# Optimization experiments

Measured on AMD Instinct MI355X. Metric: run time of the kernel, lower is better.

The kernel has to match this reference:

```python
import jax, jax.numpy as jnp
import numpy as np

N = 8192
D_IN = 1024
D_OUT = 1024


def setup_inputs() -> dict:
    key = jax.random.key(0)
    ks = jax.random.split(key, 7)
    s = 1.0 / np.sqrt(D_IN)
    return {
        "feat": jax.random.normal(ks[0], (N, D_IN), dtype=jnp.float32),
        "Wq": jax.random.uniform(ks[1], (D_IN, D_OUT), jnp.float32, -s, s),
        "bq": jax.random.uniform(ks[2], (D_OUT,), jnp.float32, -s, s),
        "Wk": jax.random.uniform(ks[3], (D_IN, D_OUT), jnp.float32, -s, s),
        "bk": jax.random.uniform(ks[4], (D_OUT,), jnp.float32, -s, s),
        "Wv": jax.random.uniform(ks[5], (D_IN, D_OUT), jnp.float32, -s, s),
        "bv": jax.random.uniform(ks[6], (D_OUT,), jnp.float32, -s, s),
    }


def reference(feat, Wq, bq, Wk, bk, Wv, bv):
    # eval mode: dropout(p=0.3, training=False) is identity
    q = feat @ Wq + bq          # [N, D_OUT]
    k = feat @ Wk + bk          # [N, D_OUT]
    v = feat @ Wv + bv          # [N, D_OUT]
    scale = 1.0 / jnp.sqrt(jnp.float32(D_OUT))
    scores = (q @ k.T) * scale  # [N, N]
    attn = jax.nn.softmax(scores, axis=1)
    return attn @ v             # [N, D_OUT]
```

## Files before the change

### kernel.cpp

```cpp
#include <hip/hip_runtime.h>
#include <hip/hip_bf16.h>
#include <stdint.h>

typedef __hip_bfloat16 bf16;
typedef __attribute__((ext_vector_type(8))) short short8;
typedef __attribute__((ext_vector_type(4))) float f32x4;

#define BM 128
#define BN 128

__device__ __forceinline__ unsigned short f2bf_bits(float x) {
    return __builtin_bit_cast(unsigned short, __float2bfloat16(x));
}

__device__ __forceinline__ void gload_lds16(const bf16* g, bf16* l) {
    __builtin_amdgcn_global_load_lds(
        (const __attribute__((address_space(1))) void*)(const void*)g,
        (__attribute__((address_space(3))) void*)(void*)l,
        16, 0, 0);
}

__global__ void cvt_f32_bf16_x4(const float* __restrict__ in, unsigned short* __restrict__ out, int n4) {
    int i = blockIdx.x * 256 + threadIdx.x;
    if (i < n4) {
        float4 v = reinterpret_cast<const float4*>(in)[i];
        ushort4 o;
        o.x = f2bf_bits(v.x); o.y = f2bf_bits(v.y);
        o.z = f2bf_bits(v.z); o.w = f2bf_bits(v.w);
        reinterpret_cast<ushort4*>(out)[i] = o;
    }
}

__global__ void wtrans_kernel(const float* __restrict__ W0, const float* __restrict__ W1,
                              const float* __restrict__ W2, bf16* __restrict__ Wt) {
    __shared__ float tile[32][33];
    const int z = blockIdx.z;
    const float* in = (z == 0) ? W0 : (z == 1) ? W1 : W2;
    bf16* out = Wt + (size_t)z * 1024 * 1024;
    const int bx = blockIdx.x, by = blockIdx.y, tx = threadIdx.x;
    for (int r = threadIdx.y; r < 32; r += 8)
        tile[r][tx] = in[(size_t)(by * 32 + r) * 1024 + bx * 32 + tx];
    __syncthreads();
    for (int r = threadIdx.y; r < 32; r += 8)
        out[(size_t)(bx * 32 + r) * 1024 + by * 32 + tx] = __float2bfloat16(tile[tx][r]);
}

__global__ void tpose_bf16(const bf16* __restrict__ in, bf16* __restrict__ out, int rows, int cols) {
    __shared__ bf16 tile[32][33];
    const int bx = blockIdx.x, by = blockIdx.y, tx = threadIdx.x;
    for (int r = threadIdx.y; r < 32; r += 8)
        tile[r][tx] = in[(size_t)(by * 32 + r) * cols + bx * 32 + tx];
    __syncthreads();
    for (int r = threadIdx.y; r < 32; r += 8)
        out[(size_t)(bx * 32 + r) * rows + by * 32 + tx] = tile[tx][r];
}

__global__ void scale_rows(float* __restrict__ out, const float* __restrict__ lsum) {
    int i = blockIdx.x * 256 + threadIdx.x;
    float4 v = reinterpret_cast<float4*>(out)[i];
    float inv = 1.0f / lsum[i >> 8];
    v.x *= inv; v.y *= inv; v.z *= inv; v.w *= inv;
    reinterpret_cast<float4*>(out)[i] = v;
}

template <int MODE, int KH>
__global__ __launch_bounds__(256, 2)
void gemm_bt(const bf16* __restrict__ A, const bf16* __restrict__ B,
             const float* __restrict__ b0, const float* __restrict__ b1,
             const float* __restrict__ b2, float* __restrict__ lsum,
             bf16* __restrict__ outb, float* __restrict__ outf,
             int M, int N, int K, int ldb, int ldout, float scale) {
    constexpr int BKT  = KH * 32;
    constexpr int TILE = 128 * 32;
    constexpr int SELEMS = (2 * KH * TILE < 9216) ? 9216 : 2 * KH * TILE;
    __shared__ bf16 smem[SELEMS];
    bf16* As = smem;
    bf16* Bs = smem + KH * TILE;

    const int tid  = threadIdx.x;
    const int lane = tid & 63;
    const int wave = tid >> 6;
    const int wm = wave & 1, wn = wave >> 1;
    const int l16  = lane & 15;
    const int quad = lane >> 4;
    const long bm0 = (long)blockIdx.x * BM;
    const long bn0 = (long)blockIdx.y * BN;

    const float* bias = nullptr;
    if (MODE == 0) {
        const int z = blockIdx.z;
        B    += (size_t)z * N * K;
        outb += (size_t)z * M * ldout;
        bias  = (z == 0) ? b0 : (z == 1) ? b1 : b2;
    }

    const int lrow = lane >> 2;
    const int lcol = (lane & 3) * 8;
    const bf16* gA[2][KH];
    const bf16* gB[2][KH];
    bf16* lA[2][KH];
    bf16* lB[2][KH];
#pragma unroll
    for (int u = 0; u < 2; u++)
#pragma unroll
        for (int h = 0; h < KH; h++) {
            gA[u][h] = A + (size_t)(bm0 + wave * 32 + u * 16 + lrow) * K + h * 32 + lcol;
            gB[u][h] = B + (size_t)(bn0 + wave * 32 + u * 16 + lrow) * ldb + h * 32 + lcol;
            lA[u][h] = As + h * TILE + (wave * 32 + u * 16) * 32;
            lB[u][h] = Bs + h * TILE + (wave * 32 + u * 16) * 32;
        }

    const bf16* Ard = As + (wm * 64 + l16) * 32 + quad * 8;
    const bf16* Brd = Bs + (wn * 64 + l16) * 32 + quad * 8;

    f32x4 acc[4][4];
    const f32x4 zero = {0.f, 0.f, 0.f, 0.f};
#pragma unroll
    for (int i = 0; i < 4; i++)
#pragma unroll
        for (int j = 0; j < 4; j++) acc[i][j] = zero;

    for (int k0 = 0; k0 < K; k0 += BKT) {
        __syncthreads();
#pragma unroll
        for (int u = 0; u < 2; u++)
#pragma unroll
            for (int h = 0; h < KH; h++) {
                gload_lds16(gA[u][h] + k0, lA[u][h]);
                gload_lds16(gB[u][h] + k0, lB[u][h]);
            }
        __syncthreads();
#pragma unroll
        for (int h = 0; h < KH; h++) {
            short8 af[4], bfr[4];
#pragma unroll
            for (int mi = 0; mi < 4; mi++)
                af[mi] = *reinterpret_cast<const short8*>(Ard + h * TILE + mi * 16 * 32);
#pragma unroll
            for (int ni = 0; ni < 4; ni++)
                bfr[ni] = *reinterpret_cast<const short8*>(Brd + h * TILE + ni * 16 * 32);
#pragma unroll
            for (int mi = 0; mi < 4; mi++)
#pragma unroll
                for (int ni = 0; ni < 4; ni++)
                    acc[mi][ni] = __builtin_amdgcn_mfma_f32_16x16x32_bf16(af[mi], bfr[ni], acc[mi][ni], 0, 0, 0);
        }
    }

    if (MODE == 0 || MODE == 1) {
        __syncthreads();
        bf16* eb = smem + wave * 1152;
        float bcol[4];
        if (MODE == 0) {
#pragma unroll
            for (int ni = 0; ni < 4; ni++) bcol[ni] = bias[bn0 + wn * 64 + l16 + ni * 16];
        }
#pragma unroll
        for (int mi = 0; mi < 4; mi++) {
#pragma unroll
            for (int r = 0; r < 4; r++) {
                float s = 0.f;
#pragma unroll
                for (int ni = 0; ni < 4; ni++) {
                    float v = acc[mi][ni][r];
                    if (MODE == 0) v += bcol[ni];
                    else { v = __expf(v * scale); s += v; }
                    eb[(quad * 4 + r) * 72 + ni * 16 + l16] = __float2bfloat16(v);
                }
                if (MODE == 1) {
                    s += __shfl_xor(s, 1);
                    s += __shfl_xor(s, 2);
                    s += __shfl_xor(s, 4);
                    s += __shfl_xor(s, 8);
                    if (l16 == 0) atomicAdd(&lsum[bm0 + wm * 64 + mi * 16 + quad * 4 + r], s);
                }
            }
            asm volatile("s_waitcnt lgkmcnt(0)" ::: "memory");
#pragma unroll
            for (int p = 0; p < 2; p++) {
                int r2 = p * 8 + (lane >> 3);
                int c2 = (lane & 7) * 8;
                short8 val = *reinterpret_cast<const short8*>(eb + r2 * 72 + c2);
                *reinterpret_cast<short8*>(
                    outb + (size_t)(bm0 + wm * 64 + mi * 16 + r2) * ldout + bn0 + wn * 64 + c2) = val;
            }
            asm volatile("s_waitcnt lgkmcnt(0)" ::: "memory");
        }
    } else {
        const int rb2 = wm * 64 + quad * 4;
        const int cb2 = wn * 64 + l16;
#pragma unroll
        for (int mi = 0; mi < 4; mi++)
#pragma unroll
            for (int r = 0; r < 4; r++) {
                long row = bm0 + rb2 + mi * 16 + r;
                float mul = (MODE == 3) ? 1.0f / lsum[row] : 0.f;
#pragma unroll
                for (int ni = 0; ni < 4; ni++) {
                    long col = bn0 + cb2 + ni * 16;
                    if (MODE == 3) outf[row * ldout + col] = acc[mi][ni][r] * mul;
                    else           outf[row * ldout + col] += acc[mi][ni][r];
                }
            }
    }
}

extern "C" void kernel_launch(void* const* d_in, const int* in_sizes, int n_in,
                              void* d_out, int out_size, void* d_ws, size_t ws_size,
                              hipStream_t stream) {
    const float* feat = (const float*)d_in[0];
    const float* Wq   = (const float*)d_in[1];
    const float* bqv  = (const float*)d_in[2];
    const float* Wk   = (const float*)d_in[3];
    const float* bkv  = (const float*)d_in[4];
    const float* Wv   = (const float*)d_in[5];
    const float* bvv  = (const float*)d_in[6];
    float* outp = (float*)d_out;

    const int M = 8192, D = 1024;
    char* ws = (char*)d_ws;
    size_t off = 0;
    auto carve = [&](size_t bytes) -> char* {
        char* r = ws + off;
        off += (bytes + 255) & ~(size_t)255;
        return r;
    };
    bf16* featb = (bf16*)carve((size_t)M * D * 2);
    bf16* Wbt   = (bf16*)carve((size_t)3 * D * D * 2);
    bf16* qkv   = (bf16*)carve((size_t)3 * M * D * 2);
    float* lsum = (float*)carve((size_t)M * 4);
    bf16* vbt   = featb;
    size_t avail = (ws_size > off) ? ws_size - off : 0;

    int C;
    if      (avail >= (size_t)M * M * 2)    C = M;
    else if (avail >= (size_t)M * 4096 * 2) C = 4096;
    else if (avail >= (size_t)M * 2048 * 2) C = 2048;
    else                                    C = 1024;
    bf16* Pc = (bf16*)carve((size_t)M * C * 2);

    {
        int n4 = M * D / 4;
        cvt_f32_bf16_x4<<<dim3((n4 + 255) / 256), dim3(256), 0, stream>>>(feat, (unsigned short*)featb, n4);
    }
    wtrans_kernel<<<dim3(32, 32, 3), dim3(32, 8), 0, stream>>>(Wq, Wk, Wv, Wbt);
    gemm_bt<0, 1><<<dim3(M / 128, D / 128, 3), dim3(256), 0, stream>>>(
        featb, Wbt, bqv, bkv, bvv, nullptr, qkv, nullptr, M, D, D, D, D, 1.0f);
    tpose_bf16<<<dim3(D / 32, M / 32), dim3(32, 8), 0, stream>>>(qkv + (size_t)2 * M * D, vbt, M, D);
    hipMemsetAsync(lsum, 0, (size_t)M * 4, stream);

    const float scale = 0.03125f;
    bf16* qb = qkv;
    bf16* kb = qkv + (size_t)M * D;
    if (C == M) {
        gemm_bt<1, 1><<<dim3(M / 128, M / 128), dim3(256), 0, stream>>>(
            qb, kb, nullptr, nullptr, nullptr, lsum, Pc, nullptr, M, M, D, D, M, scale);
        gemm_bt<3, 2><<<dim3(M / 128, D / 128), dim3(256), 0, stream>>>(
            Pc, vbt, nullptr, nullptr, nullptr, lsum, nullptr, outp, M, D, M, M, D, 0.f);
    } else {
        hipMemsetAsync(outp, 0, (size_t)M * D * 4, stream);
        for (int c = 0; c < M / C; c++) {
            gemm_bt<1, 1><<<dim3(M / 128, C / 128), dim3(256), 0, stream>>>(
                qb, kb + (size_t)c * C * D, nullptr, nullptr, nullptr, lsum, Pc, nullptr,
                M, C, D, D, C, scale);
            gemm_bt<2, 2><<<dim3(M / 128, D / 128), dim3(256), 0, stream>>>(
                Pc, vbt + (size_t)c * C, nullptr, nullptr, nullptr, nullptr, nullptr, outp,
                M, D, C, M, D, 0.f);
        }
        scale_rows<<<dim3(M * D / 4 / 256), dim3(256), 0, stream>>>(outp, lsum);
    }
}
```

Baseline: 477.5 us.

## Compute Q·K^T scores with FP8 MFMA, storing Q and K as FP8

The QKV projection now writes Q and K as FP8 (e4m3) instead of bf16, and a new kernel computes the N×N score GEMM with the scaled 16x16x128 f8f6f4 MFMA. Exp, row-sum and bf16 output are fused into its epilogue as before. This aims to halve operand bytes and double matrix throughput for the largest GEMM. The cost is lower precision in the attention scores, which could hurt accuracy given unscaled FP8 conversion.

```diff
diff --git a/kernel.cpp b/kernel.cpp
--- a/kernel.cpp
+++ b/kernel.cpp
@@ -5,6 +5,7 @@
 typedef __hip_bfloat16 bf16;
 typedef __attribute__((ext_vector_type(8))) short short8;
 typedef __attribute__((ext_vector_type(4))) float f32x4;
+typedef __attribute__((ext_vector_type(8))) int i32x8;
 
 #define BM 128
 #define BN 128
@@ -13,11 +14,24 @@
     return __builtin_bit_cast(unsigned short, __float2bfloat16(x));
 }
 
-__device__ __forceinline__ void gload_lds16(const bf16* g, bf16* l) {
+__device__ __forceinline__ float bfbits2f(unsigned short b) {
+    return __builtin_bit_cast(float, (unsigned)b << 16);
+}
+
+__device__ __forceinline__ void gload_lds16(const void* g, void* l) {
     __builtin_amdgcn_global_load_lds(
-        (const __attribute__((address_space(1))) void*)(const void*)g,
-        (__attribute__((address_space(3))) void*)(void*)l,
+        (const __attribute__((address_space(1))) void*)g,
+        (__attribute__((address_space(3))) void*)l,
         16, 0, 0);
+}
+
+__device__ __forceinline__ i32x8 ldfrag32(const uint8_t* p) {
+    int4 a = *reinterpret_cast<const int4*>(p);
+    int4 b = *reinterpret_cast<const int4*>(p + 16);
+    i32x8 r;
+    r[0] = a.x; r[1] = a.y; r[2] = a.z; r[3] = a.w;
+    r[4] = b.x; r[5] = b.y; r[6] = b.z; r[7] = b.w;
+    return r;
 }
 
 __global__ void cvt_f32_bf16_x4(const float* __restrict__ in, unsigned short* __restrict__ out, int n4) {
@@ -69,8 +83,8 @@
              const float* __restrict__ b0, const float* __restrict__ b1,
              const float* __restrict__ b2, float* __restrict__ lsum,
              bf16* __restrict__ outb, float* __restrict__ outf,
+             uint8_t* __restrict__ qk8,
              int M, int N, int K, int ldb, int ldout, float scale) {
-    constexpr int BKT  = KH * 32;
     constexpr int TILE = 128 * 32;
     constexpr int SELEMS = (2 * KH * TILE < 9216) ? 9216 : 2 * KH * TILE;
     __shared__ bf16 smem[SELEMS];
@@ -87,11 +101,11 @@
     const long bn0 = (long)blockIdx.y * BN;
 
     const float* bias = nullptr;
+    int z = 0;
     if (MODE == 0) {
-        const int z = blockIdx.z;
-        B    += (size_t)z * N * K;
-        outb += (size_t)z * M * ldout;
-        bias  = (z == 0) ? b0 : (z == 1) ? b1 : b2;
+        z = blockIdx.z;
+        B   += (size_t)z * N * K;
+        bias = (z == 0) ? b0 : (z == 1) ? b1 : b2;
     }
 
     const int lrow = lane >> 2;
@@ -120,7 +134,7 @@
 #pragma unroll
         for (int j = 0; j < 4; j++) acc[i][j] = zero;
 
-    for (int k0 = 0; k0 < K; k0 += BKT) {
+    for (int k0 = 0; k0 < K; k0 += KH * 32) {
         __syncthreads();
 #pragma unroll
         for (int u = 0; u < 2; u++)
@@ -147,42 +161,43 @@
         }
     }
 
-    if (MODE == 0 || MODE == 1) {
+    if (MODE == 0) {
         __syncthreads();
         bf16* eb = smem + wave * 1152;
         float bcol[4];
-        if (MODE == 0) {
-#pragma unroll
-            for (int ni = 0; ni < 4; ni++) bcol[ni] = bias[bn0 + wn * 64 + l16 + ni * 16];
-        }
+#pragma unroll
+        for (int ni = 0; ni < 4; ni++) bcol[ni] = bias[bn0 + wn * 64 + l16 + ni * 16];
 #pragma unroll
         for (int mi = 0; mi < 4; mi++) {
 #pragma unroll
-            for (int r = 0; r < 4; r++) {
-                float s = 0.f;
-#pragma unroll
-                for (int ni = 0; ni < 4; ni++) {
-                    float v = acc[mi][ni][r];
-                    if (MODE == 0) v += bcol[ni];
-                    else { v = __expf(v * scale); s += v; }
-                    eb[(quad * 4 + r) * 72 + ni * 16 + l16] = __float2bfloat16(v);
-                }
-                if (MODE == 1) {
-                    s += __shfl_xor(s, 1);
-                    s += __shfl_xor(s, 2);
-                    s += __shfl_xor(s, 4);
-                    s += __shfl_xor(s, 8);
-                    if (l16 == 0) atomicAdd(&lsum[bm0 + wm * 64 + mi * 16 + quad * 4 + r], s);
-                }
-            }
+            for (int r = 0; r < 4; r++)
+#pragma unroll
+                for (int ni = 0; ni < 4; ni++)
+                    eb[(quad * 4 + r) * 72 + ni * 16 + l16] =
+                        __float2bfloat16(acc[mi][ni][r] + bcol[ni]);
             asm volatile("s_waitcnt lgkmcnt(0)" ::: "memory");
 #pragma unroll
             for (int p = 0; p < 2; p++) {
                 int r2 = p * 8 + (lane >> 3);
                 int c2 = (lane & 7) * 8;
                 short8 val = *reinterpret_cast<const short8*>(eb + r2 * 72 + c2);
-                *reinterpret_cast<short8*>(
-                    outb + (size_t)(bm0 + wm * 64 + mi * 16 + r2) * ldout + bn0 + wn * 64 + c2) = val;
+                long row = bm0 + wm * 64 + mi * 16 + r2;
+                long col = bn0 + wn * 64 + c2;
+                if (z < 2) {
+                    unsigned lo = 0, hi = 0;
+                    lo = __builtin_amdgcn_cvt_pk_fp8_f32(bfbits2f((unsigned short)val[0]),
+                                                         bfbits2f((unsigned short)val[1]), lo, false);
+                    lo = __builtin_amdgcn_cvt_pk_fp8_f32(bfbits2f((unsigned short)val[2]),
+                                                         bfbits2f((unsigned short)val[3]), lo, true);
+                    hi = __builtin_amdgcn_cvt_pk_fp8_f32(bfbits2f((unsigned short)val[4]),
+                                                         bfbits2f((unsigned short)val[5]), hi, false);
+                    hi = __builtin_amdgcn_cvt_pk_fp8_f32(bfbits2f((unsigned short)val[6]),
+                                                         bfbits2f((unsigned short)val[7]), hi, true);
+                    int2 o; o.x = (int)lo; o.y = (int)hi;
+                    *reinterpret_cast<int2*>(qk8 + (size_t)z * M * ldout + row * ldout + col) = o;
+                } else {
+                    *reinterpret_cast<short8*>(outb + row * (size_t)ldout + col) = val;
+                }
             }
             asm volatile("s_waitcnt lgkmcnt(0)" ::: "memory");
         }
@@ -202,6 +217,106 @@
                     else           outf[row * ldout + col] += acc[mi][ni][r];
                 }
             }
+    }
+}
+
+__global__ __launch_bounds__(256, 2)
+void gemm_s_fp8(const uint8_t* __restrict__ A, const uint8_t* __restrict__ B,
+                float* __restrict__ lsum, bf16* __restrict__ outb,
+                int ldout, float scale) {
+    __shared__ uint8_t smem[32768];
+    uint8_t* As = smem;
+    uint8_t* Bs = smem + 16384;
+
+    const int tid  = threadIdx.x;
+    const int lane = tid & 63;
+    const int wave = tid >> 6;
+    const int wm = wave & 1, wn = wave >> 1;
+    const int l16  = lane & 15;
+    const int quad = lane >> 4;
+    const long bm0 = (long)blockIdx.x * BM;
+    const long bn0 = (long)blockIdx.y * BN;
+
+    const int lrow = lane >> 2;
+    const int lcol = (lane & 3) * 16;
+    const uint8_t* gA[2][2];
+    const uint8_t* gB[2][2];
+    uint8_t* lA[2][2];
+    uint8_t* lB[2][2];
+#pragma unroll
+    for (int u = 0; u < 2; u++)
+#pragma unroll
+        for (int h = 0; h < 2; h++) {
+            gA[u][h] = A + (size_t)(bm0 + wave * 32 + u * 16 + lrow) * 1024 + h * 64 + lcol;
+            gB[u][h] = B + (size_t)(bn0 + wave * 32 + u * 16 + lrow) * 1024 + h * 64 + lcol;
+            lA[u][h] = As + h * 8192 + (wave * 32 + u * 16) * 64;
+            lB[u][h] = Bs + h * 8192 + (wave * 32 + u * 16) * 64;
+        }
+
+    const uint8_t* Ard = As + (quad >> 1) * 8192 + (wm * 64 + l16) * 64 + (quad & 1) * 32;
+    const uint8_t* Brd = Bs + (quad >> 1) * 8192 + (wn * 64 + l16) * 64 + (quad & 1) * 32;
+
+    f32x4 acc[4][4];
+    const f32x4 zero = {0.f, 0.f, 0.f, 0.f};
+#pragma unroll
+    for (int i = 0; i < 4; i++)
+#pragma unroll
+        for (int j = 0; j < 4; j++) acc[i][j] = zero;
+
+    for (int k0 = 0; k0 < 1024; k0 += 128) {
+        __syncthreads();
+#pragma unroll
+        for (int u = 0; u < 2; u++)
+#pragma unroll
+            for (int h = 0; h < 2; h++) {
+                gload_lds16(gA[u][h] + k0, lA[u][h]);
+                gload_lds16(gB[u][h] + k0, lB[u][h]);
+            }
+        __syncthreads();
+        i32x8 af[4], bfr[4];
+#pragma unroll
+        for (int mi = 0; mi < 4; mi++)
+            af[mi] = ldfrag32(Ard + mi * 16 * 64);
+#pragma unroll
+        for (int ni = 0; ni < 4; ni++)
+            bfr[ni] = ldfrag32(Brd + ni * 16 * 64);
+#pragma unroll
+        for (int mi = 0; mi < 4; mi++)
+#pragma unroll
+            for (int ni = 0; ni < 4; ni++)
+                acc[mi][ni] = __builtin_amdgcn_mfma_scale_f32_16x16x128_f8f6f4(
+                    af[mi], bfr[ni], acc[mi][ni], 0, 0, 0, 0x7F7F7F7F, 0, 0x7F7F7F7F);
+    }
+
+    __syncthreads();
+    bf16* eb = reinterpret_cast<bf16*>(smem) + wave * 1152;
+#pragma unroll
+    for (int mi = 0; mi < 4; mi++) {
+#pragma unroll
+        for (int r = 0; r < 4; r++) {
+            float s = 0.f;
+#pragma unroll
+            for (int ni = 0; ni < 4; ni++) {
+                float e = __expf(acc[mi][ni][r] * scale);
+                s += e;
+                eb[(quad * 4 + r) * 72 + ni * 16 + l16] = __float2bfloat16(e);
+            }
+            s += __shfl_xor(s, 1);
+            s += __shfl_xor(s, 2);
+            s += __shfl_xor(s, 4);
+            s += __shfl_xor(s, 8);
+            if (l16 == 0) atomicAdd(&lsum[bm0 + wm * 64 + mi * 16 + quad * 4 + r], s);
+        }
+        asm volatile("s_waitcnt lgkmcnt(0)" ::: "memory");
+#pragma unroll
+        for (int p = 0; p < 2; p++) {
+            int r2 = p * 8 + (lane >> 3);
+            int c2 = (lane & 7) * 8;
+            short8 val = *reinterpret_cast<const short8*>(eb + r2 * 72 + c2);
+            *reinterpret_cast<short8*>(
+                outb + (size_t)(bm0 + wm * 64 + mi * 16 + r2) * ldout + bn0 + wn * 64 + c2) = val;
+        }
+        asm volatile("s_waitcnt lgkmcnt(0)" ::: "memory");
     }
 }
 
@@ -225,11 +340,12 @@
         off += (bytes + 255) & ~(size_t)255;
         return r;
     };
-    bf16* featb = (bf16*)carve((size_t)M * D * 2);
-    bf16* Wbt   = (bf16*)carve((size_t)3 * D * D * 2);
-    bf16* qkv   = (bf16*)carve((size_t)3 * M * D * 2);
-    float* lsum = (float*)carve((size_t)M * 4);
-    bf16* vbt   = featb;
+    bf16* featb   = (bf16*)carve((size_t)M * D * 2);
+    bf16* Wbt     = (bf16*)carve((size_t)3 * D * D * 2);
+    uint8_t* qk8  = (uint8_t*)carve((size_t)2 * M * D);
+    bf16* vb      = (bf16*)carve((size_t)M * D * 2);
+    float* lsum   = (float*)carve((size_t)M * 4);
+    bf16* vbt     = featb;
     size_t avail = (ws_size > off) ? ws_size - off : 0;
 
     int C;
@@ -245,26 +361,26 @@
     }
     wtrans_kernel<<<dim3(32, 32, 3), dim3(32, 8), 0, stream>>>(Wq, Wk, Wv, Wbt);
     gemm_bt<0, 1><<<dim3(M / 128, D / 128, 3), dim3(256), 0, stream>>>(
-        featb, Wbt, bqv, bkv, bvv, nullptr, qkv, nullptr, M, D, D, D, D, 1.0f);
-    tpose_bf16<<<dim3(D / 32, M / 32), dim3(32, 8), 0, stream>>>(qkv + (size_t)2 * M * D, vbt, M, D);
+        featb, Wbt, bqv, bkv, bvv, nullptr, vb, nullptr, qk8, M, D, D, D, D, 1.0f);
+    tpose_bf16<<<dim3(D / 32, M / 32), dim3(32, 8), 0, stream>>>(vb, vbt, M, D);
     hipMemsetAsync(lsum, 0, (size_t)M * 4, stream);
 
     const float scale = 0.03125f;
-    bf16* qb = qkv;
-    bf16* kb = qkv + (size_t)M * D;
+    const uint8_t* q8 = qk8;
+    const uint8_t* k8 = qk8 + (size_t)M * D;
     if (C == M) {
-        gemm_bt<1, 1><<<dim3(M / 128, M / 128), dim3(256), 0, stream>>>(
-            qb, kb, nullptr, nullptr, nullptr, lsum, Pc, nullptr, M, M, D, D, M, scale);
+        gemm_s_fp8<<<dim3(M / 128, M / 128), dim3(256), 0, stream>>>(
+            q8, k8, lsum, Pc, M, scale);
         gemm_bt<3, 2><<<dim3(M / 128, D / 128), dim3(256), 0, stream>>>(
-            Pc, vbt, nullptr, nullptr, nullptr, lsum, nullptr, outp, M, D, M, M, D, 0.f);
+            Pc, vbt, nullptr, nullptr, nullptr, lsum, nullptr, outp, nullptr,
+            M, D, M, M, D, 0.f);
     } else {
         hipMemsetAsync(outp, 0, (size_t)M * D * 4, stream);
         for (int c = 0; c < M / C; c++) {
-            gemm_bt<1, 1><<<dim3(M / 128, C / 128), dim3(256), 0, stream>>>(
-                qb, kb + (size_t)c * C * D, nullptr, nullptr, nullptr, lsum, Pc, nullptr,
-                M, C, D, D, C, scale);
+            gemm_s_fp8<<<dim3(M / 128, C / 128), dim3(256), 0, stream>>>(
+                q8, k8 + (size_t)c * C * D, lsum, Pc, C, scale);
             gemm_bt<2, 2><<<dim3(M / 128, D / 128), dim3(256), 0, stream>>>(
-                Pc, vbt + (size_t)c * C, nullptr, nullptr, nullptr, nullptr, nullptr, outp,
+                Pc, vbt + (size_t)c * C, nullptr, nullptr, nullptr, nullptr, nullptr, outp, nullptr,
                 M, D, C, M, D, 0.f);
         }
         scale_rows<<<dim3(M * D / 4 / 256), dim3(256), 0, stream>>>(outp, lsum);
```

Measured after the change: 864.5 us. 1.81x slower.
